# Kernel tuning notes

Hardware: AMD Instinct MI355X
Metric: run time of the kernel (lower is better)

The kernel has to match this reference:

```python
import jax, jax.numpy as jnp
import numpy as np

KINEMATIC_CHAIN = [[0,2,5,8,11],[0,1,4,7,10],[0,3,6,9,12,15],[9,14,17,19,21],[9,13,16,18,20]]
_paths = [c[1:] for c in KINEMATIC_CHAIN]
SEG_S = np.array([p[i] for p in _paths for i in range(len(p)-1)])      # [16] segment start joints
SEG_E = np.array([p[i+1] for p in _paths for i in range(len(p)-1)])    # [16] segment end joints
PATH_ID = np.array([k for k, p in enumerate(_paths) for _ in range(len(p)-1)])
N_PATHS = len(_paths)
P_ONEHOT = (PATH_ID[:, None] == np.arange(N_PATHS)[None, :]).astype(np.float32)  # [16,5]


def _safe_normalize(v):
    ss = jnp.sum(v * v, axis=-1, keepdims=True)
    return jnp.where(ss > 0, v / jnp.sqrt(jnp.where(ss > 0, ss, 1.0)), 0.0)


def _gli_pairwise(s1, e1, s2, e2):
    # all inputs broadcast to [..., 3]; returns Gauss linking integral per segment pair
    r13, r14 = s2 - s1, e2 - s1
    r23, r24 = s2 - e1, e2 - e1
    r12, r34 = e1 - s1, e2 - s2
    f0 = _safe_normalize(jnp.cross(r13, r14))
    f1 = _safe_normalize(jnp.cross(r14, r24))
    f2 = _safe_normalize(jnp.cross(r24, r23))
    f3 = _safe_normalize(jnp.cross(r23, r13))
    def asin_dot(a, b):
        return jnp.arcsin(jnp.clip(jnp.sum(a * b, -1), -1.0, 1.0))
    total = asin_dot(f0, f1) + asin_dot(f1, f2) + asin_dot(f2, f3) + asin_dot(f3, f0)
    sign = jnp.sum(jnp.cross(r34, r12) * r13, -1)
    mult = jnp.where(sign <= 0, -1.0, 1.0)
    return mult * total / (4.0 * jnp.pi)


def _bbox_xz(m):
    x, z = m[..., 0], m[..., 2]
    return x.min(-1), x.max(-1), z.min(-1), z.max(-1)


def setup_inputs() -> dict:
    key = jax.random.key(0)
    k1, k2 = jax.random.split(key)
    B, F, J = 64, 240, 22
    motion1 = jax.random.normal(k1, (B, F, J, 3), dtype=jnp.float32)
    motion2 = jax.random.normal(k2, (B, F, J, 3), dtype=jnp.float32)
    return {"motion1": motion1, "motion2": motion2}


def reference(motion1, motion2):
    B, F = motion1.shape[0], motion1.shape[1]
    P = jnp.asarray(P_ONEHOT, motion1.dtype)
    # gather all 16 skeleton segments, broadcast to 16x16 segment pairs
    s1 = motion1[..., SEG_S, :][..., :, None, :]   # [B,F,16,1,3]
    e1 = motion1[..., SEG_E, :][..., :, None, :]
    s2 = motion2[..., SEG_S, :][..., None, :, :]   # [B,F,1,16,3]
    e2 = motion2[..., SEG_E, :][..., None, :, :]
    gli_seg = _gli_pairwise(s1, e1, s2, e2)        # [B,F,16,16]
    # sum segment-pair GLIs into path-pair blocks -> [B,F,5,5]
    gli_pose = jnp.einsum('bfmn,mi,nj->bfij', gli_seg, P, P)

    # xz bounding-box overlap per frame, then dilate by 1 frame (window start-1..end+1)
    nx1, xx1, nz1, xz1 = _bbox_xz(motion1)
    nx2, xx2, nz2, xz2 = _bbox_xz(motion2)
    flag = (xx1 >= nx2) & (xx2 >= nx1) & (xz1 >= nz2) & (xz2 >= nz1)   # [B,F]
    pad = jnp.zeros_like(flag[:, :1])
    mask = flag | jnp.concatenate([flag[:, 1:], pad], 1) | jnp.concatenate([pad, flag[:, :-1]], 1)
    gli_motion = gli_pose * mask[..., None, None].astype(gli_pose.dtype)

    vel = jnp.abs(gli_motion[:, 1:] - gli_motion[:, :-1]).reshape(B, F - 1, -1)
    return vel.max(-1)
```

## Files before the change

kernel.cpp:

```cpp
#include <hip/hip_runtime.h>
#include <math.h>

#define BB 64
#define FF 240
#define NJ 22
#define NFRM (BB * FF)

#define PK8(a0,a1,a2,a3,a4,a5,a6,a7) \
  (  (unsigned long long)(a0)        | ((unsigned long long)(a1) << 5)  \
   | ((unsigned long long)(a2) << 10)| ((unsigned long long)(a3) << 15) \
   | ((unsigned long long)(a4) << 20)| ((unsigned long long)(a5) << 25) \
   | ((unsigned long long)(a6) << 30)| ((unsigned long long)(a7) << 35) )
static constexpr unsigned long long SEG_S_LO = PK8(2,5,8,1,4,7,3,6);
static constexpr unsigned long long SEG_S_HI = PK8(9,12,14,17,19,13,16,18);
static constexpr unsigned long long SEG_E_LO = PK8(5,8,11,4,7,10,6,9);
static constexpr unsigned long long SEG_E_HI = PK8(12,15,17,19,21,16,18,20);
static constexpr unsigned PO_PK = 0u | (3u<<5) | (6u<<10) | (10u<<15) | (13u<<20);
static constexpr unsigned PC_PK = 3u | (3u<<5) | (4u<<10) | (3u<<15)  | (3u<<20);

__device__ __forceinline__ int seg_start(int m){
    unsigned long long p = (m < 8) ? SEG_S_LO : SEG_S_HI;
    return (int)((p >> ((m & 7) * 5)) & 31);
}
__device__ __forceinline__ int seg_end(int m){
    unsigned long long p = (m < 8) ? SEG_E_LO : SEG_E_HI;
    return (int)((p >> ((m & 7) * 5)) & 31);
}

typedef float v2 __attribute__((ext_vector_type(2)));
__device__ __forceinline__ v2 vset(float a){ v2 r; r.x = a; r.y = a; return r; }
__device__ __forceinline__ v2 vfma(v2 a, v2 b, v2 c){ return __builtin_elementwise_fma(a, b, c); }

struct V3p { v2 x, y, z; };
__device__ __forceinline__ V3p subp(V3p a, V3p b){ return {a.x-b.x, a.y-b.y, a.z-b.z}; }
__device__ __forceinline__ V3p crsp(V3p a, V3p b){
    return { vfma(a.y, b.z, -(a.z*b.y)), vfma(a.z, b.x, -(a.x*b.z)), vfma(a.x, b.y, -(a.y*b.x)) };
}
__device__ __forceinline__ v2 dtp(V3p a, V3p b){ return vfma(a.x, b.x, vfma(a.y, b.y, a.z*b.z)); }
__device__ __forceinline__ v2 clamp1p(v2 d){
    return __builtin_elementwise_min(__builtin_elementwise_max(d, vset(-1.0f)), vset(1.0f));
}
__device__ __forceinline__ v2 asin_fast2(v2 d){
    v2 ax = __builtin_elementwise_abs(d);
    v2 p = vfma(vfma(vfma(vset(-0.0187293f), ax, vset(0.0742610f)), ax, vset(-0.2121144f)),
                ax, vset(1.5707288f));
    v2 om = vset(1.0f) - ax;
    v2 s; s.x = __builtin_amdgcn_sqrtf(om.x); s.y = __builtin_amdgcn_sqrtf(om.y);
    v2 r = vset(1.57079632679f) - s * p;
    return __builtin_elementwise_copysign(r, d);
}

__global__ void __launch_bounds__(256, 3) k_main(const float* __restrict__ m1,
                                                 const float* __restrict__ m2,
                                                 float* __restrict__ gp,
                                                 int* __restrict__ flags){
    __shared__ __align__(8) float pts[4][2][136];
    __shared__ float g[4][2][256];
    __shared__ float ext[4][2][8];
    int tid = threadIdx.x;
    int w = tid >> 6, lane = tid & 63;
    int fr0 = blockIdx.x * 8 + w * 2;

    const float2* gs1 = (const float2*)(m1 + (size_t)fr0 * 66);
    const float2* gs2 = (const float2*)(m2 + (size_t)fr0 * 66);
    for (int u = lane; u < 132; u += 64){
        bool a = u < 66;
        int v = a ? u : u - 66;
        ((float2*)pts[w][a ? 0 : 1])[v] = (a ? gs1 : gs2)[v];
    }
    __syncthreads();

    if (lane < 16){
        int f = lane >> 3;
        int sel = lane & 7;
        int mot = sel >> 2;
        int c = sel & 2;
        bool mx = sel & 1;
        const float* P = &pts[w][mot][f * 66];
        float a = 1e30f;
        #pragma unroll
        for (int j = 0; j < NJ; ++j){
            float v = P[j*3 + c];
            a = fminf(a, mx ? -v : v);
        }
        ext[w][f][sel] = mx ? -a : a;
    }

    int n = lane & 15, q = lane >> 4;
    const float* P1 = pts[w][0];
    const float* P2 = pts[w][1];
    int js2 = seg_start(n) * 3, je2 = seg_end(n) * 3;
    V3p s2 = { v2{P2[js2  ], P2[66+js2  ]},
               v2{P2[js2+1], P2[66+js2+1]},
               v2{P2[js2+2], P2[66+js2+2]} };
    V3p e2 = { v2{P2[je2  ], P2[66+je2  ]},
               v2{P2[je2+1], P2[66+je2+1]},
               v2{P2[je2+2], P2[66+je2+2]} };

    V3p s1v[4], e1v[4];
    #pragma unroll
    for (int k = 0; k < 4; ++k){
        int m = q + 4 * k;
        int js1 = seg_start(m) * 3, je1 = seg_end(m) * 3;
        s1v[k] = { v2{P1[js1  ], P1[66+js1  ]},
                   v2{P1[js1+1], P1[66+js1+1]},
                   v2{P1[js1+2], P1[66+js1+2]} };
        e1v[k] = { v2{P1[je1  ], P1[66+je1  ]},
                   v2{P1[je1+1], P1[66+je1+1]},
                   v2{P1[je1+2], P1[66+je1+2]} };
    }

    #pragma unroll
    for (int k = 0; k < 4; ++k){
        V3p r13 = subp(s2, s1v[k]), r14 = subp(e2, s1v[k]);
        V3p r23 = subp(s2, e1v[k]), r24 = subp(e2, e1v[k]);
        V3p f0 = crsp(r13, r14);
        V3p f1 = crsp(r14, r24);
        V3p f2 = crsp(r24, r23);
        V3p f3 = crsp(r23, r13);
        v2 ss0 = dtp(f0,f0), ss1 = dtp(f1,f1), ss2 = dtp(f2,f2), ss3 = dtp(f3,f3);
        v2 rd01 = dtp(f0,f1), rd12 = dtp(f1,f2);
        v2 rd23 = dtp(f2,f3), rd30 = dtp(f3,f0);
        v2 q01 = ss0*ss1, q12 = ss1*ss2, q23 = ss2*ss3, q30 = ss3*ss0;
        v2 sg = dtp(f3, r14);

        v2 i01, i12, i23, i30;
        i01.x = rsqrtf(fmaxf(q01.x, 1e-30f));
        i01.y = rsqrtf(fmaxf(q01.y, 1e-30f));
        i12.x = rsqrtf(fmaxf(q12.x, 1e-30f));
        i12.y = rsqrtf(fmaxf(q12.y, 1e-30f));
        i23.x = rsqrtf(fmaxf(q23.x, 1e-30f));
        i23.y = rsqrtf(fmaxf(q23.y, 1e-30f));
        i30.x = rsqrtf(fmaxf(q30.x, 1e-30f));
        i30.y = rsqrtf(fmaxf(q30.y, 1e-30f));

        v2 t = asin_fast2(clamp1p(rd01 * i01))
             + asin_fast2(clamp1p(rd12 * i12))
             + asin_fast2(clamp1p(rd23 * i23))
             + asin_fast2(clamp1p(rd30 * i30));
        float r0 = (sg.x >= 0.0f ? -t.x : t.x) * 0.07957747154594767f;
        float r1 = (sg.y >= 0.0f ? -t.y : t.y) * 0.07957747154594767f;
        g[w][0][(k << 6) | lane] = r0;
        g[w][1][(k << 6) | lane] = r1;
    }
    __syncthreads();

    if (lane < 50){
        int f = lane >= 25 ? 1 : 0;
        int pp = lane - f * 25;
        int i = pp / 5, j = pp - i * 5;
        int poi = (int)((PO_PK >> (i*5)) & 31), pci = (int)((PC_PK >> (i*5)) & 31);
        int poj = (int)((PO_PK >> (j*5)) & 31), pcj = (int)((PC_PK >> (j*5)) & 31);
        float s = 0.0f;
        for (int a = 0; a < pci; ++a)
            for (int b = 0; b < pcj; ++b)
                s += g[w][f][(poi + a) * 16 + (poj + b)];
        int fr = fr0 + f;
        int bb = fr / FF, ff = fr - bb * FF;
        gp[((size_t)bb * 25 + pp) * FF + ff] = s;
    } else if (lane < 52){
        int f = lane - 50;
        const float* e = ext[w][f];
        flags[fr0 + f] = (e[1] >= e[4] && e[5] >= e[0] &&
                          e[3] >= e[6] && e[7] >= e[2]) ? 1 : 0;
    }
}

__global__ void __launch_bounds__(64) k_vel(const float* __restrict__ gp,
                                            const int* __restrict__ flags,
                                            float* __restrict__ out){
    int b = blockIdx.x >> 2;
    int f = ((blockIdx.x & 3) << 6) | threadIdx.x;
    if (f >= FF - 1) return;
    const int* fl = flags + b * FF;

    int vc = fl[f] | fl[f + 1];
    int v0 = vc;
    if (f > 0) v0 |= fl[f - 1];
    float mk0 = v0 ? 1.0f : 0.0f;

    int v1 = vc;
    if (f + 2 < FF) v1 |= fl[f + 2];
    float mk1 = v1 ? 1.0f : 0.0f;

    const float* gb = gp + (size_t)b * 25 * FF + f;
    float mx = 0.0f;
    #pragma unroll
    for (int p = 0; p < 25; ++p){
        float g0 = gb[p * FF];
        float g1 = gb[p * FF + 1];
        float d = fabsf(g1 * mk1 - g0 * mk0);
        mx = fmaxf(mx, d);
    }
    out[b * (FF - 1) + f] = mx;
}

extern "C" void kernel_launch(void* const* d_in, const int* in_sizes, int n_in,
                              void* d_out, int out_size, void* d_ws, size_t ws_size,
                              hipStream_t stream) {
    const float* m1 = (const float*)d_in[0];
    const float* m2 = (const float*)d_in[1];
    float* gp    = (float*)d_ws;
    int*   flags = (int*)((char*)d_ws + (size_t)BB * 25 * FF * 4);
    float* out = (float*)d_out;

    k_main<<<NFRM / 8, 256, 0, stream>>>(m1, m2, gp, flags);
    k_vel<<<BB * 4, 64, 0, stream>>>(gp, flags, out);
}
```

Measured before the change: 75.25 us.

## Fuse GLI and velocity kernels with per-block frame chunks and halo flags

Merges the main GLI kernel and the velocity/max kernel into one launch. Each 512-thread block handles 16 frames of one batch (15 outputs with overlap), keeps the pooled path-pair sums and bbox flags in shared memory, and computes the two halo flags directly from global memory. This removes the second launch and the workspace round-trip, at the cost of recomputing one overlapping frame per chunk plus two halo bbox computations, and of leaving a mostly idle final phase in which only 15 threads work.

```diff
diff --git a/kernel.cpp b/kernel.cpp
--- a/kernel.cpp
+++ b/kernel.cpp
@@ -5,6 +5,9 @@
 #define FF 240
 #define NJ 22
 #define NFRM (BB * FF)
+
+#define NCH 16
+#define CH_OUT 15
 
 #define PK8(a0,a1,a2,a3,a4,a5,a6,a7) \
   (  (unsigned long long)(a0)        | ((unsigned long long)(a1) << 5)  \
@@ -50,23 +53,32 @@
     return __builtin_elementwise_copysign(r, d);
 }
 
-__global__ void __launch_bounds__(256, 3) k_main(const float* __restrict__ m1,
-                                                 const float* __restrict__ m2,
-                                                 float* __restrict__ gp,
-                                                 int* __restrict__ flags){
-    __shared__ __align__(8) float pts[4][2][136];
-    __shared__ float g[4][2][256];
-    __shared__ float ext[4][2][8];
+__global__ void __launch_bounds__(512) k_fused(const float* __restrict__ m1,
+                                               const float* __restrict__ m2,
+                                               float* __restrict__ out){
+    __shared__ __align__(8) float pts[8][2][136];
+    __shared__ float g[8][2][256];
+    __shared__ float ext[8][2][8];
+    __shared__ float gsum[16][26];
+    __shared__ int   flg[18];
+
     int tid = threadIdx.x;
     int w = tid >> 6, lane = tid & 63;
-    int fr0 = blockIdx.x * 8 + w * 2;
-
-    const float2* gs1 = (const float2*)(m1 + (size_t)fr0 * 66);
-    const float2* gs2 = (const float2*)(m2 + (size_t)fr0 * 66);
+    int b = blockIdx.x >> 4;
+    int c = blockIdx.x & (NCH - 1);
+    int fbase = c * CH_OUT;
+    int fl0 = fbase + 2 * w;
+    int fl1 = fl0 + 1;
+    int gF0 = b * FF + (fl0 < FF - 1 ? fl0 : FF - 1);
+    int gF1 = b * FF + (fl1 < FF - 1 ? fl1 : FF - 1);
+
     for (int u = lane; u < 132; u += 64){
-        bool a = u < 66;
-        int v = a ? u : u - 66;
-        ((float2*)pts[w][a ? 0 : 1])[v] = (a ? gs1 : gs2)[v];
+        int mot  = (u >= 66) ? 1 : 0;
+        int v    = u - 66 * mot;
+        int fsel = (v >= 33) ? 1 : 0;
+        int idx  = v - 33 * fsel;
+        const float* src = (mot ? m2 : m1) + (size_t)(fsel ? gF1 : gF0) * 66;
+        ((float2*)pts[w][mot])[v] = ((const float2*)src)[idx];
     }
     __syncthreads();
 
@@ -74,16 +86,34 @@
         int f = lane >> 3;
         int sel = lane & 7;
         int mot = sel >> 2;
-        int c = sel & 2;
+        int cc = sel & 2;
         bool mx = sel & 1;
         const float* P = &pts[w][mot][f * 66];
         float a = 1e30f;
         #pragma unroll
         for (int j = 0; j < NJ; ++j){
-            float v = P[j*3 + c];
+            float v = P[j*3 + cc];
             a = fminf(a, mx ? -v : v);
         }
         ext[w][f][sel] = mx ? -a : a;
+    } else if (w == 0 && lane < 18){
+        int h = lane - 16;
+        int hf = h ? fbase + 16 : fbase - 1;
+        hf = hf < 0 ? 0 : (hf > FF - 1 ? FF - 1 : hf);
+        const float* q1 = m1 + ((size_t)b * FF + hf) * 66;
+        const float* q2 = m2 + ((size_t)b * FF + hf) * 66;
+        float nx1 = 1e30f, xx1 = -1e30f, nz1 = 1e30f, xz1 = -1e30f;
+        float nx2 = 1e30f, xx2 = -1e30f, nz2 = 1e30f, xz2 = -1e30f;
+        #pragma unroll
+        for (int j = 0; j < NJ; ++j){
+            float x1 = q1[j*3], z1 = q1[j*3+2];
+            float x2 = q2[j*3], z2 = q2[j*3+2];
+            nx1 = fminf(nx1, x1); xx1 = fmaxf(xx1, x1);
+            nz1 = fminf(nz1, z1); xz1 = fmaxf(xz1, z1);
+            nx2 = fminf(nx2, x2); xx2 = fmaxf(xx2, x2);
+            nz2 = fminf(nz2, z2); xz2 = fmaxf(xz2, z2);
+        }
+        flg[h ? 17 : 0] = (xx1 >= nx2 && xx2 >= nx1 && xz1 >= nz2 && xz2 >= nz1) ? 1 : 0;
     }
 
     int n = lane & 15, q = lane >> 4;
@@ -153,46 +183,36 @@
         int poj = (int)((PO_PK >> (j*5)) & 31), pcj = (int)((PC_PK >> (j*5)) & 31);
         float s = 0.0f;
         for (int a = 0; a < pci; ++a)
-            for (int b = 0; b < pcj; ++b)
-                s += g[w][f][(poi + a) * 16 + (poj + b)];
-        int fr = fr0 + f;
-        int bb = fr / FF, ff = fr - bb * FF;
-        gp[((size_t)bb * 25 + pp) * FF + ff] = s;
+            for (int bb2 = 0; bb2 < pcj; ++bb2)
+                s += g[w][f][(poi + a) * 16 + (poj + bb2)];
+        gsum[2 * w + f][pp] = s;
     } else if (lane < 52){
         int f = lane - 50;
         const float* e = ext[w][f];
-        flags[fr0 + f] = (e[1] >= e[4] && e[5] >= e[0] &&
-                          e[3] >= e[6] && e[7] >= e[2]) ? 1 : 0;
-    }
-}
-
-__global__ void __launch_bounds__(64) k_vel(const float* __restrict__ gp,
-                                            const int* __restrict__ flags,
-                                            float* __restrict__ out){
-    int b = blockIdx.x >> 2;
-    int f = ((blockIdx.x & 3) << 6) | threadIdx.x;
-    if (f >= FF - 1) return;
-    const int* fl = flags + b * FF;
-
-    int vc = fl[f] | fl[f + 1];
-    int v0 = vc;
-    if (f > 0) v0 |= fl[f - 1];
-    float mk0 = v0 ? 1.0f : 0.0f;
-
-    int v1 = vc;
-    if (f + 2 < FF) v1 |= fl[f + 2];
-    float mk1 = v1 ? 1.0f : 0.0f;
-
-    const float* gb = gp + (size_t)b * 25 * FF + f;
-    float mx = 0.0f;
-    #pragma unroll
-    for (int p = 0; p < 25; ++p){
-        float g0 = gb[p * FF];
-        float g1 = gb[p * FF + 1];
-        float d = fabsf(g1 * mk1 - g0 * mk0);
-        mx = fmaxf(mx, d);
-    }
-    out[b * (FF - 1) + f] = mx;
+        flg[2 * w + f + 1] = (e[1] >= e[4] && e[5] >= e[0] &&
+                              e[3] >= e[6] && e[7] >= e[2]) ? 1 : 0;
+    }
+    __syncthreads();
+
+    if (tid < CH_OUT){
+        int f_rel = tid;
+        int f_out = fbase + f_rel;
+        if (f_out < FF - 1){
+            int m0 = flg[f_rel + 1] | flg[f_rel + 2];
+            if (f_out > 0) m0 |= flg[f_rel];
+            int m1v = flg[f_rel + 1] | flg[f_rel + 2];
+            if (f_out + 2 < FF) m1v |= flg[f_rel + 3];
+            float mk0 = m0 ? 1.0f : 0.0f;
+            float mk1 = m1v ? 1.0f : 0.0f;
+            float mx = 0.0f;
+            #pragma unroll
+            for (int p = 0; p < 25; ++p){
+                float d = fabsf(gsum[f_rel + 1][p] * mk1 - gsum[f_rel][p] * mk0);
+                mx = fmaxf(mx, d);
+            }
+            out[b * (FF - 1) + f_out] = mx;
+        }
+    }
 }
 
 extern "C" void kernel_launch(void* const* d_in, const int* in_sizes, int n_in,
@@ -200,10 +220,8 @@
                               hipStream_t stream) {
     const float* m1 = (const float*)d_in[0];
     const float* m2 = (const float*)d_in[1];
-    float* gp    = (float*)d_ws;
-    int*   flags = (int*)((char*)d_ws + (size_t)BB * 25 * FF * 4);
     float* out = (float*)d_out;
-
-    k_main<<<NFRM / 8, 256, 0, stream>>>(m1, m2, gp, flags);
-    k_vel<<<BB * 4, 64, 0, stream>>>(gp, flags, out);
-}
+    (void)d_ws; (void)ws_size;
+
+    k_fused<<<BB * NCH, 512, 0, stream>>>(m1, m2, out);
+}
```

Result: no change. 75.08 us (-0.2%).
